# Optimization experiments

Measured on AMD Instinct MI355X. Metric: run time of the kernel, lower is better.

Reference implementation:

```python
import jax, jax.numpy as jnp
import numpy as np

N, D_IN, D_OUT, Q_DIM = 4096, 256, 256, 64


def _xavier(key, shape):
    fan_in, fan_out = shape[-2], shape[-1]
    bound = float(np.sqrt(6.0 / (fan_in + fan_out)))
    return jax.random.uniform(key, shape, jnp.float32, -bound, bound)


def setup_inputs() -> dict:
    key = jax.random.key(0)
    k_x, k_q, k_w, k_b = jax.random.split(key, 4)
    x = jax.random.normal(k_x, (N, D_IN), jnp.float32)
    query_vectors = jax.random.normal(k_q, (N, Q_DIM), jnp.float32)
    W_1 = _xavier(k_w, (Q_DIM, D_IN, D_OUT))  # xavier over last two dims (matches torch on 3D)
    b_1 = _xavier(k_b, (Q_DIM, D_OUT))
    return {"x": x, "query_vectors": query_vectors, "W_1": W_1, "b_1": b_1}


def reference(x, query_vectors, W_1, b_1):
    # Per-sample dynamic weight: W[n] = sum_d q[n,d] * W_1[d]; then x[n] @ W[n] + q[n] @ b_1.
    # Fused single contraction avoids materializing the [n, i, o] tensor; same math.
    out = jnp.einsum('ni,nd,dio->no', x, query_vectors, W_1)
    out = out + query_vectors @ b_1
    return out
```

## Files before the change

kernel.cpp:

```cpp
#include <hip/hip_runtime.h>
#include <stdint.h>


typedef _Float16 f16;
typedef f16 f16x8 __attribute__((ext_vector_type(8)));
typedef float f32x16 __attribute__((ext_vector_type(16)));

#define QDIM 64

#define XFRAG(DST, PTR)                                      \
  do {                                                       \
    float4 a_ = *(const float4*)(PTR);                       \
    float4 b_ = *(const float4*)((PTR) + 4);                 \
    f16x8 h_;                                                \
    h_[0] = (f16)a_.x; h_[1] = (f16)a_.y; h_[2] = (f16)a_.z; \
    h_[3] = (f16)a_.w; h_[4] = (f16)b_.x; h_[5] = (f16)b_.y; \
    h_[6] = (f16)b_.z; h_[7] = (f16)b_.w;                    \
    DST = h_;                                                \
  } while (0)

__global__ __launch_bounds__(256) void prep(const float* __restrict__ W,
                                            const float* __restrict__ B1,
                                            const float* __restrict__ X,
                                            f16* __restrict__ Wt,
                                            f16* __restrict__ Xt,
                                            f16* __restrict__ Bt) {
  const int b = blockIdx.x, t = threadIdx.x;
  if (b < 512) {
    const int d = b >> 3, grp = b & 7;
    const int ibL = t >> 6;
    const int ib = (grp << 2) + ibL;
    const int o0 = (t & 63) << 2;
    const int ic = ib >> 1, hb = ib & 1;
    float v[32];
#pragma unroll
    for (int j = 0; j < 8; ++j) {
      float4 f = *(const float4*)(W + ((size_t)d * 256 + (ib << 3) + j) * 256 + o0);
      v[j * 4 + 0] = f.x; v[j * 4 + 1] = f.y;
      v[j * 4 + 2] = f.z; v[j * 4 + 3] = f.w;
    }
#pragma unroll
    for (int oo = 0; oo < 4; ++oo) {
      const int o = o0 + oo, ncb = o >> 5, c = o & 31;
      f16x8 h;
#pragma unroll
      for (int j = 0; j < 8; ++j) h[j] = (f16)v[j * 4 + oo];
      *(f16x8*)((char*)Wt + ((((size_t)ncb * 64 + d) * 16 + ic) << 10) +
                (hb << 9) + (c << 4)) = h;
    }
  } else if (b < 576) {
    const int mb = b - 512;
#pragma unroll
    for (int rep = 0; rep < 8; ++rep) {
      const int u = (rep << 8) + t;
      const int row = u & 63, ish = u >> 6;
      const float* src = X + ((size_t)((mb << 6) + row)) * 256 + (ish << 3);
      f16x8 h;
      XFRAG(h, src);
      *(f16x8*)((char*)Xt + ((((size_t)mb * 16 + (ish >> 1)) * 2 + (ish & 1)) << 10) +
                (row << 4)) = h;
    }
  } else {
#pragma unroll
    for (int kb = 0; kb < 8; ++kb) {
      const float* src = B1 + ((size_t)kb << 3) * 256 + t;
      f16x8 h;
#pragma unroll
      for (int j = 0; j < 8; ++j) h[j] = (f16)src[(size_t)j << 8];
      *(f16x8*)((char*)Bt + (((size_t)(t >> 5) * 4 + (kb >> 1)) << 10) +
                ((kb & 1) << 9) + ((t & 31) << 4)) = h;
    }
  }
}

__global__ __launch_bounds__(256, 4) void mlp_main(const float* __restrict__ Q,
                                                   const f16* __restrict__ Wt,
                                                   const f16* __restrict__ Xt,
                                                   const f16* __restrict__ Bt,
                                                   float* __restrict__ out) {
  __shared__ __align__(16) float red[4][32][36];

  const int bid = blockIdx.x;
  const int nc = bid & 7;
  const int mb = bid >> 3;
  const int t = threadIdx.x;
  const int w = t >> 6;
  const int l = t & 63;
  const int l31 = l & 31;
  const int hf = l >> 5;

  const char* wl = (const char*)Wt + (((size_t)(nc * 64 + (w << 4))) << 14) +
                   (hf << 9) + (l31 << 4);
  const char* xb = (const char*)Xt + ((size_t)(mb >> 1) << 15) + (hf << 10) +
                   ((size_t)(((mb & 1) << 5) + l31) << 4);

  f16 qr[16];
  {
    const float* qp = Q + ((size_t)((mb << 5) + l31)) * QDIM + (w << 4);
#pragma unroll
    for (int g = 0; g < 4; ++g) {
      float4 v = *(const float4*)(qp + (g << 2));
      qr[g * 4 + 0] = (f16)v.x; qr[g * 4 + 1] = (f16)v.y;
      qr[g * 4 + 2] = (f16)v.z; qr[g * 4 + 3] = (f16)v.w;
    }
  }

  f32x16 acc[2];
#pragma unroll
  for (int p = 0; p < 2; ++p)
#pragma unroll
    for (int r = 0; r < 16; ++r) acc[p][r] = 0.f;

  f16x8 Wr[8], xfA, xfB;

  const int icoff = (((mb & 7) << 1) | (((mb >> 5) & 1) << 3)) & 15;

  xfA = *(const f16x8*)(xb + ((size_t)icoff << 11));
#pragma unroll
  for (int i = 0; i < 8; ++i)
    Wr[i] = *(const f16x8*)(wl + (((size_t)(i * 16 + icoff)) << 10));

  for (int s = 0; s < 16; ++s) {
    const int ic = (icoff + s) & 15;
    const int icn = (icoff + s + 1) & 15;
    xfB = *(const f16x8*)(xb + ((size_t)icn << 11));
#pragma unroll
    for (int i = 0; i < 8; ++i) {
      f16x8 wfr = Wr[i];
      Wr[i] = *(const f16x8*)(wl + (((size_t)((8 + i) * 16 + ic)) << 10));
      f16x8 a = xfA * qr[i];
      acc[i & 1] = __builtin_amdgcn_mfma_f32_32x32x16_f16(a, wfr, acc[i & 1], 0, 0, 0);
    }
#pragma unroll
    for (int i = 0; i < 8; ++i) {
      f16x8 wfr = Wr[i];
      Wr[i] = *(const f16x8*)(wl + (((size_t)(i * 16 + icn)) << 10));
      f16x8 a = xfA * qr[8 + i];
      acc[i & 1] = __builtin_amdgcn_mfma_f32_32x32x16_f16(a, wfr, acc[i & 1], 0, 0, 0);
    }
    xfA = xfB;
  }

#pragma unroll
  for (int r = 0; r < 16; ++r) acc[0][r] += acc[1][r];

  if (w == 0) {
#pragma unroll
    for (int kc = 0; kc < 4; ++kc) {
      f16x8 bf = *(const f16x8*)((const char*)Bt +
          (((size_t)nc * 4 + kc) << 10) + (hf << 9) + (l31 << 4));
      f16x8 q0;
      XFRAG(q0, Q + ((size_t)((mb << 5) + l31)) * QDIM + (kc << 4) + (hf << 3));
      acc[0] = __builtin_amdgcn_mfma_f32_32x32x16_f16(q0, bf, acc[0], 0, 0, 0);
    }
  }

#pragma unroll
  for (int r = 0; r < 16; ++r) {
    const int row0 = (r & 3) + ((r >> 2) << 3) + (hf << 2);
    red[w][row0][l31] = acc[0][r];
  }
  __syncthreads();

  const int row = t >> 3;
  const int cg = (t & 7) << 2;
  float4 sum = {0.f, 0.f, 0.f, 0.f};
#pragma unroll
  for (int wq = 0; wq < 4; ++wq) {
    float4 v = *(const float4*)(&red[wq][row][cg]);
    sum.x += v.x; sum.y += v.y; sum.z += v.z; sum.w += v.w;
  }
  *(float4*)(out + ((size_t)((mb << 5) + row)) * 256 + (nc << 5) + cg) = sum;
}

extern "C" void kernel_launch(void* const* d_in, const int* in_sizes, int n_in,
                              void* d_out, int out_size, void* d_ws, size_t ws_size,
                              hipStream_t stream) {
  (void)in_sizes; (void)n_in; (void)out_size; (void)ws_size;
  const float* x  = (const float*)d_in[0];
  const float* q  = (const float*)d_in[1];
  const float* W1 = (const float*)d_in[2];
  const float* b1 = (const float*)d_in[3];
  float* out = (float*)d_out;

  f16* Wt = (f16*)d_ws;
  f16* Bt = (f16*)((char*)d_ws + ((size_t)8 << 20));
  f16* Xt = (f16*)((char*)d_ws + ((size_t)8 << 20) + 32768);

  prep<<<577, 256, 0, stream>>>(W1, b1, x, Wt, Xt, Bt);
  mlp_main<<<1024, 256, 0, stream>>>(q, Wt, Xt, Bt, out);
}
```

Measured before the change: 133.1 us.

## Enlarge blocks to 1024 threads and reuse weight fragments across four row tiles

```diff
diff --git a/kernel.cpp b/kernel.cpp
--- a/kernel.cpp
+++ b/kernel.cpp
@@ -73,12 +73,12 @@
   }
 }
 
-__global__ __launch_bounds__(256, 4) void mlp_main(const float* __restrict__ Q,
-                                                   const f16* __restrict__ Wt,
-                                                   const f16* __restrict__ Xt,
-                                                   const f16* __restrict__ Bt,
-                                                   float* __restrict__ out) {
-  __shared__ __align__(16) float red[4][32][36];
+__global__ __launch_bounds__(1024, 4) void mlp_main(const float* __restrict__ Q,
+                                                    const f16* __restrict__ Wt,
+                                                    const f16* __restrict__ Xt,
+                                                    const f16* __restrict__ Bt,
+                                                    float* __restrict__ out) {
+  __shared__ __align__(16) float red[8][128][36];
 
   const int bid = blockIdx.x;
   const int nc = bid & 7;
@@ -89,88 +89,101 @@
   const int l31 = l & 31;
   const int hf = l >> 5;
 
-  const char* wl = (const char*)Wt + (((size_t)(nc * 64 + (w << 4))) << 14) +
+  const char* wl = (const char*)Wt + (((size_t)(nc * 64 + (w << 2))) << 14) +
                    (hf << 9) + (l31 << 4);
-  const char* xb = (const char*)Xt + ((size_t)(mb >> 1) << 15) + (hf << 10) +
-                   ((size_t)(((mb & 1) << 5) + l31) << 4);
-
-  f16 qr[16];
-  {
-    const float* qp = Q + ((size_t)((mb << 5) + l31)) * QDIM + (w << 4);
-#pragma unroll
-    for (int g = 0; g < 4; ++g) {
-      float4 v = *(const float4*)(qp + (g << 2));
-      qr[g * 4 + 0] = (f16)v.x; qr[g * 4 + 1] = (f16)v.y;
-      qr[g * 4 + 2] = (f16)v.z; qr[g * 4 + 3] = (f16)v.w;
-    }
-  }
-
-  f32x16 acc[2];
-#pragma unroll
-  for (int p = 0; p < 2; ++p)
-#pragma unroll
-    for (int r = 0; r < 16; ++r) acc[p][r] = 0.f;
-
-  f16x8 Wr[8], xfA, xfB;
-
-  const int icoff = (((mb & 7) << 1) | (((mb >> 5) & 1) << 3)) & 15;
-
-  xfA = *(const f16x8*)(xb + ((size_t)icoff << 11));
-#pragma unroll
-  for (int i = 0; i < 8; ++i)
-    Wr[i] = *(const f16x8*)(wl + (((size_t)(i * 16 + icoff)) << 10));
+  const char* xB = (const char*)Xt + ((size_t)(mb << 1) << 15) + (hf << 10) +
+                   ((size_t)l31 << 4);
+
+  f16 qr[4][4];
+#pragma unroll
+  for (int mt = 0; mt < 4; ++mt) {
+    float4 qv = *(const float4*)(Q + (size_t)((mb << 7) + (mt << 5) + l31) * QDIM +
+                                 (w << 2));
+    qr[mt][0] = (f16)qv.x; qr[mt][1] = (f16)qv.y;
+    qr[mt][2] = (f16)qv.z; qr[mt][3] = (f16)qv.w;
+  }
+
+  f32x16 acc[4];
+#pragma unroll
+  for (int mt = 0; mt < 4; ++mt)
+#pragma unroll
+    for (int r = 0; r < 16; ++r) acc[mt][r] = 0.f;
+
+  f16x8 Wr[4], xfA[4];
+
+  const int icoff = (mb & 7) << 1;
+
+#pragma unroll
+  for (int dd = 0; dd < 4; ++dd)
+    Wr[dd] = *(const f16x8*)(wl + (((size_t)((dd << 4) + icoff)) << 10));
+#pragma unroll
+  for (int mt = 0; mt < 4; ++mt)
+    xfA[mt] = *(const f16x8*)(xB + ((mt >> 1) << 15) + ((mt & 1) << 9) +
+                              ((size_t)icoff << 11));
 
   for (int s = 0; s < 16; ++s) {
-    const int ic = (icoff + s) & 15;
     const int icn = (icoff + s + 1) & 15;
-    xfB = *(const f16x8*)(xb + ((size_t)icn << 11));
-#pragma unroll
-    for (int i = 0; i < 8; ++i) {
-      f16x8 wfr = Wr[i];
-      Wr[i] = *(const f16x8*)(wl + (((size_t)((8 + i) * 16 + ic)) << 10));
-      f16x8 a = xfA * qr[i];
-      acc[i & 1] = __builtin_amdgcn_mfma_f32_32x32x16_f16(a, wfr, acc[i & 1], 0, 0, 0);
-    }
-#pragma unroll
-    for (int i = 0; i < 8; ++i) {
-      f16x8 wfr = Wr[i];
-      Wr[i] = *(const f16x8*)(wl + (((size_t)(i * 16 + icn)) << 10));
-      f16x8 a = xfA * qr[8 + i];
-      acc[i & 1] = __builtin_amdgcn_mfma_f32_32x32x16_f16(a, wfr, acc[i & 1], 0, 0, 0);
-    }
-    xfA = xfB;
-  }
-
-#pragma unroll
-  for (int r = 0; r < 16; ++r) acc[0][r] += acc[1][r];
-
-  if (w == 0) {
+#pragma unroll
+    for (int dd = 0; dd < 4; ++dd) {
+      f16x8 wf = Wr[dd];
+      Wr[dd] = *(const f16x8*)(wl + (((size_t)((dd << 4) + icn)) << 10));
+#pragma unroll
+      for (int mt = 0; mt < 4; ++mt) {
+        f16x8 a = xfA[mt] * qr[mt][dd];
+        acc[mt] = __builtin_amdgcn_mfma_f32_32x32x16_f16(a, wf, acc[mt], 0, 0, 0);
+      }
+    }
+#pragma unroll
+    for (int mt = 0; mt < 4; ++mt)
+      xfA[mt] = *(const f16x8*)(xB + ((mt >> 1) << 15) + ((mt & 1) << 9) +
+                                ((size_t)icn << 11));
+  }
+
+  if (w == 15) {
 #pragma unroll
     for (int kc = 0; kc < 4; ++kc) {
       f16x8 bf = *(const f16x8*)((const char*)Bt +
           (((size_t)nc * 4 + kc) << 10) + (hf << 9) + (l31 << 4));
-      f16x8 q0;
-      XFRAG(q0, Q + ((size_t)((mb << 5) + l31)) * QDIM + (kc << 4) + (hf << 3));
-      acc[0] = __builtin_amdgcn_mfma_f32_32x32x16_f16(q0, bf, acc[0], 0, 0, 0);
-    }
-  }
-
-#pragma unroll
-  for (int r = 0; r < 16; ++r) {
-    const int row0 = (r & 3) + ((r >> 2) << 3) + (hf << 2);
-    red[w][row0][l31] = acc[0][r];
+#pragma unroll
+      for (int mt = 0; mt < 4; ++mt) {
+        f16x8 qf;
+        XFRAG(qf, Q + (size_t)((mb << 7) + (mt << 5) + l31) * QDIM +
+                  (kc << 4) + (hf << 3));
+        acc[mt] = __builtin_amdgcn_mfma_f32_32x32x16_f16(qf, bf, acc[mt], 0, 0, 0);
+      }
+    }
+  }
+
+  if (w < 8) {
+#pragma unroll
+    for (int mt = 0; mt < 4; ++mt)
+#pragma unroll
+      for (int r = 0; r < 16; ++r) {
+        const int row = (mt << 5) + (r & 3) + ((r >> 2) << 3) + (hf << 2);
+        red[w][row][l31] = acc[mt][r];
+      }
   }
   __syncthreads();
-
-  const int row = t >> 3;
-  const int cg = (t & 7) << 2;
-  float4 sum = {0.f, 0.f, 0.f, 0.f};
-#pragma unroll
-  for (int wq = 0; wq < 4; ++wq) {
-    float4 v = *(const float4*)(&red[wq][row][cg]);
-    sum.x += v.x; sum.y += v.y; sum.z += v.z; sum.w += v.w;
-  }
-  *(float4*)(out + ((size_t)((mb << 5) + row)) * 256 + (nc << 5) + cg) = sum;
+  if (w >= 8) {
+#pragma unroll
+    for (int mt = 0; mt < 4; ++mt)
+#pragma unroll
+      for (int r = 0; r < 16; ++r) {
+        const int row = (mt << 5) + (r & 3) + ((r >> 2) << 3) + (hf << 2);
+        red[w - 8][row][l31] += acc[mt][r];
+      }
+  }
+  __syncthreads();
+
+  const int r = t >> 3;
+  const int c0 = (t & 7) << 2;
+  float4 s4 = {0.f, 0.f, 0.f, 0.f};
+#pragma unroll
+  for (int j = 0; j < 8; ++j) {
+    float4 v = *(const float4*)(&red[j][r][c0]);
+    s4.x += v.x; s4.y += v.y; s4.z += v.z; s4.w += v.w;
+  }
+  *(float4*)(out + ((size_t)((mb << 7) + r)) * 256 + (nc << 5) + c0) = s4;
 }
 
 extern "C" void kernel_launch(void* const* d_in, const int* in_sizes, int n_in,
@@ -188,5 +201,5 @@
   f16* Xt = (f16*)((char*)d_ws + ((size_t)8 << 20) + 32768);
 
   prep<<<577, 256, 0, stream>>>(W1, b1, x, Wt, Xt, Bt);
-  mlp_main<<<1024, 256, 0, stream>>>(q, Wt, Xt, Bt, out);
+  mlp_main<<<256, 1024, 0, stream>>>(q, Wt, Xt, Bt, out);
 }
```

New measurement: 402.4 us. 202% more time.

## Split Q-dim reduction across blocks with LDS-staged W tiles and separate reduce

Applied to the files above, without the earlier changes.

```diff
diff --git a/kernel.cpp b/kernel.cpp
--- a/kernel.cpp
+++ b/kernel.cpp
@@ -7,6 +7,13 @@
 typedef float f32x16 __attribute__((ext_vector_type(16)));
 
 #define QDIM 64
+
+__device__ __forceinline__ void gl_lds16(const void* g, void* s) {
+  __builtin_amdgcn_global_load_lds(
+      (const __attribute__((address_space(1))) void*)(uintptr_t)g,
+      (__attribute__((address_space(3))) void*)(uint32_t)(uintptr_t)s,
+      16, 0, 0);
+}
 
 #define XFRAG(DST, PTR)                                      \
   do {                                                       \
@@ -28,24 +35,18 @@
   const int b = blockIdx.x, t = threadIdx.x;
   if (b < 512) {
     const int d = b >> 3, grp = b & 7;
-    const int ibL = t >> 6;
-    const int ib = (grp << 2) + ibL;
-    const int o0 = (t & 63) << 2;
-    const int ic = ib >> 1, hb = ib & 1;
-    float v[32];
-#pragma unroll
-    for (int j = 0; j < 8; ++j) {
-      float4 f = *(const float4*)(W + ((size_t)d * 256 + (ib << 3) + j) * 256 + o0);
-      v[j * 4 + 0] = f.x; v[j * 4 + 1] = f.y;
-      v[j * 4 + 2] = f.z; v[j * 4 + 3] = f.w;
-    }
-#pragma unroll
-    for (int oo = 0; oo < 4; ++oo) {
-      const int o = o0 + oo, ncb = o >> 5, c = o & 31;
+#pragma unroll
+    for (int r = 0; r < 4; ++r) {
+      const int u = (r << 8) + t;
+      const int ibq = u >> 8;
+      const int o = u & 255;
+      const int ib = (grp << 2) + ibq;
       f16x8 h;
 #pragma unroll
-      for (int j = 0; j < 8; ++j) h[j] = (f16)v[j * 4 + oo];
-      *(f16x8*)((char*)Wt + ((((size_t)ncb * 64 + d) * 16 + ic) << 10) +
+      for (int j = 0; j < 8; ++j)
+        h[j] = (f16)W[((size_t)d * 256 + (ib << 3) + j) * 256 + o];
+      const int ncg = o >> 5, c = o & 31, ic = ib >> 1, hb = ib & 1;
+      *(f16x8*)((char*)Wt + ((((size_t)ncg * 64 + d) * 16 + ic) << 10) +
                 (hb << 9) + (c << 4)) = h;
     }
   } else if (b < 576) {
@@ -73,104 +74,141 @@
   }
 }
 
-__global__ __launch_bounds__(256, 4) void mlp_main(const float* __restrict__ Q,
+__global__ __launch_bounds__(512, 2) void mlp_main(const float* __restrict__ Q,
                                                    const f16* __restrict__ Wt,
                                                    const f16* __restrict__ Xt,
                                                    const f16* __restrict__ Bt,
-                                                   float* __restrict__ out) {
-  __shared__ __align__(16) float red[4][32][36];
+                                                   float* __restrict__ P) {
+  __shared__ __align__(16) char sw0[16384];
+  __shared__ __align__(16) char sw1[16384];
 
   const int bid = blockIdx.x;
-  const int nc = bid & 7;
-  const int mb = bid >> 3;
+  const int nc = bid & 3;
+  const int ks = (bid >> 2) & 7;
+  const int mb = bid >> 5;
   const int t = threadIdx.x;
   const int w = t >> 6;
+  const int wn = w & 1;
+  const int wm = w >> 1;
   const int l = t & 63;
   const int l31 = l & 31;
   const int hf = l >> 5;
 
-  const char* wl = (const char*)Wt + (((size_t)(nc * 64 + (w << 4))) << 14) +
-                   (hf << 9) + (l31 << 4);
-  const char* xb = (const char*)Xt + ((size_t)(mb >> 1) << 15) + (hf << 10) +
-                   ((size_t)(((mb & 1) << 5) + l31) << 4);
-
-  f16 qr[16];
+  const int dlo = ks << 3;
+  const int st = mb & 7;
+
+  const char* gW = (const char*)Wt + ((size_t)nc << 21) + (l << 4);
+
+  const char* xB = (const char*)Xt + ((size_t)((mb << 2) + wm) << 15) +
+                   (hf << 10) + (l31 << 4);
+
+  f16 qr0[8], qr1[8];
   {
-    const float* qp = Q + ((size_t)((mb << 5) + l31)) * QDIM + (w << 4);
-#pragma unroll
-    for (int g = 0; g < 4; ++g) {
-      float4 v = *(const float4*)(qp + (g << 2));
-      qr[g * 4 + 0] = (f16)v.x; qr[g * 4 + 1] = (f16)v.y;
-      qr[g * 4 + 2] = (f16)v.z; qr[g * 4 + 3] = (f16)v.w;
-    }
-  }
-
-  f32x16 acc[2];
-#pragma unroll
-  for (int p = 0; p < 2; ++p)
-#pragma unroll
-    for (int r = 0; r < 16; ++r) acc[p][r] = 0.f;
-
-  f16x8 Wr[8], xfA, xfB;
-
-  const int icoff = (((mb & 7) << 1) | (((mb >> 5) & 1) << 3)) & 15;
-
-  xfA = *(const f16x8*)(xb + ((size_t)icoff << 11));
-#pragma unroll
-  for (int i = 0; i < 8; ++i)
-    Wr[i] = *(const f16x8*)(wl + (((size_t)(i * 16 + icoff)) << 10));
-
-  for (int s = 0; s < 16; ++s) {
-    const int ic = (icoff + s) & 15;
-    const int icn = (icoff + s + 1) & 15;
-    xfB = *(const f16x8*)(xb + ((size_t)icn << 11));
-#pragma unroll
-    for (int i = 0; i < 8; ++i) {
-      f16x8 wfr = Wr[i];
-      Wr[i] = *(const f16x8*)(wl + (((size_t)((8 + i) * 16 + ic)) << 10));
-      f16x8 a = xfA * qr[i];
-      acc[i & 1] = __builtin_amdgcn_mfma_f32_32x32x16_f16(a, wfr, acc[i & 1], 0, 0, 0);
-    }
-#pragma unroll
-    for (int i = 0; i < 8; ++i) {
-      f16x8 wfr = Wr[i];
-      Wr[i] = *(const f16x8*)(wl + (((size_t)(i * 16 + icn)) << 10));
-      f16x8 a = xfA * qr[8 + i];
-      acc[i & 1] = __builtin_amdgcn_mfma_f32_32x32x16_f16(a, wfr, acc[i & 1], 0, 0, 0);
-    }
-    xfA = xfB;
-  }
-
-#pragma unroll
-  for (int r = 0; r < 16; ++r) acc[0][r] += acc[1][r];
-
-  if (w == 0) {
+    const float* qp0 = Q + ((size_t)((mb << 8) + (wm << 6) + l31)) * QDIM + dlo;
+    const float* qp1 = qp0 + (size_t)32 * QDIM;
+#pragma unroll
+    for (int dt = 0; dt < 8; ++dt) {
+      qr0[dt] = (f16)qp0[(dt + st) & 7];
+      qr1[dt] = (f16)qp1[(dt + st) & 7];
+    }
+  }
+
+  f32x16 acc0, acc1;
+#pragma unroll
+  for (int r = 0; r < 16; ++r) { acc0[r] = 0.f; acc1[r] = 0.f; }
+
+  f16x8 xf[16];
+
+#define STAGE2(H, DABS, SBUF)                                              \
+  do {                                                                     \
+    gl_lds16(gW + ((size_t)(DABS) << 14) + ((((H) << 3) + w) << 10),       \
+             (SBUF) + ((w << 1) << 10) + (l << 4));                        \
+    gl_lds16(gW + ((size_t)1 << 20) + ((size_t)(DABS) << 14) +             \
+                 ((((H) << 3) + w) << 10),                                 \
+             (SBUF) + (((w << 1) + 1) << 10) + (l << 4));                  \
+  } while (0)
+
+#define LOADXF(H)                                                          \
+  do {                                                                     \
+    _Pragma("unroll")                                                      \
+    for (int k2 = 0; k2 < 8; ++k2) {                                       \
+      xf[k2 * 2 + 0] = *(const f16x8*)(xB + ((((H) << 3) + k2) << 11));    \
+      xf[k2 * 2 + 1] =                                                     \
+          *(const f16x8*)(xB + ((((H) << 3) + k2) << 11) + (1 << 9));      \
+    }                                                                      \
+  } while (0)
+
+#define CSTEP(DT, SBUF)                                                    \
+  do {                                                                     \
+    const f16 qa_ = qr0[DT], qb_ = qr1[DT];                                \
+    _Pragma("unroll")                                                      \
+    for (int k2 = 0; k2 < 8; ++k2) {                                       \
+      f16x8 bf_ = *(const f16x8*)((SBUF) + (((k2 << 1) | wn) << 10) +      \
+                                  (l << 4));                               \
+      acc0 = __builtin_amdgcn_mfma_f32_32x32x16_f16(xf[k2 * 2 + 0] * qa_,  \
+                                                    bf_, acc0, 0, 0, 0);   \
+      acc1 = __builtin_amdgcn_mfma_f32_32x32x16_f16(xf[k2 * 2 + 1] * qb_,  \
+                                                    bf_, acc1, 0, 0, 0);   \
+    }                                                                      \
+  } while (0)
+
+  STAGE2(0, dlo + (st & 7), sw0);
+  LOADXF(0);
+  __syncthreads();
+
+#pragma unroll
+  for (int h = 0; h < 2; ++h) {
+#pragma unroll
+    for (int dt = 0; dt < 8; ++dt) {
+      const int step = (h << 3) + dt;
+      if (step < 15) {
+        const int hn = (step + 1) >> 3, dtn = (step + 1) & 7;
+        const int dabs = dlo + ((dtn + st) & 7);
+        if (step & 1) STAGE2(hn, dabs, sw0); else STAGE2(hn, dabs, sw1);
+      }
+      if (step & 1) CSTEP(dt, sw1); else CSTEP(dt, sw0);
+      __syncthreads();
+    }
+    if (h == 0) LOADXF(1);
+  }
+
+  if (ks == 0) {
+    const int ncg = (nc << 1) + wn;
 #pragma unroll
     for (int kc = 0; kc < 4; ++kc) {
       f16x8 bf = *(const f16x8*)((const char*)Bt +
-          (((size_t)nc * 4 + kc) << 10) + (hf << 9) + (l31 << 4));
-      f16x8 q0;
-      XFRAG(q0, Q + ((size_t)((mb << 5) + l31)) * QDIM + (kc << 4) + (hf << 3));
-      acc[0] = __builtin_amdgcn_mfma_f32_32x32x16_f16(q0, bf, acc[0], 0, 0, 0);
-    }
-  }
-
+          (((size_t)ncg * 4 + kc) << 10) + (hf << 9) + (l31 << 4));
+      f16x8 q0, q1;
+      XFRAG(q0, Q + ((size_t)((mb << 8) + (wm << 6) + l31)) * QDIM +
+                (kc << 4) + (hf << 3));
+      XFRAG(q1, Q + ((size_t)((mb << 8) + (wm << 6) + 32 + l31)) * QDIM +
+                (kc << 4) + (hf << 3));
+      acc0 = __builtin_amdgcn_mfma_f32_32x32x16_f16(q0, bf, acc0, 0, 0, 0);
+      acc1 = __builtin_amdgcn_mfma_f32_32x32x16_f16(q1, bf, acc1, 0, 0, 0);
+    }
+  }
+
+  float* Pg = P + ((size_t)ks << 20);
+  const int colg = (nc << 6) + (wn << 5) + l31;
+  const int rbase = (mb << 8) + (wm << 6);
 #pragma unroll
   for (int r = 0; r < 16; ++r) {
-    const int row0 = (r & 3) + ((r >> 2) << 3) + (hf << 2);
-    red[w][row0][l31] = acc[0][r];
-  }
-  __syncthreads();
-
-  const int row = t >> 3;
-  const int cg = (t & 7) << 2;
-  float4 sum = {0.f, 0.f, 0.f, 0.f};
-#pragma unroll
-  for (int wq = 0; wq < 4; ++wq) {
-    float4 v = *(const float4*)(&red[wq][row][cg]);
-    sum.x += v.x; sum.y += v.y; sum.z += v.z; sum.w += v.w;
-  }
-  *(float4*)(out + ((size_t)((mb << 5) + row)) * 256 + (nc << 5) + cg) = sum;
+    const int rr = (r & 3) + ((r >> 2) << 3) + (hf << 2);
+    Pg[(size_t)(rbase + rr) * 256 + colg] = acc0[r];
+    Pg[(size_t)(rbase + 32 + rr) * 256 + colg] = acc1[r];
+  }
+}
+
+__global__ __launch_bounds__(256) void reduce8(const float* __restrict__ P,
+                                               float* __restrict__ out) {
+  const size_t i = (((size_t)blockIdx.x << 8) + threadIdx.x) << 2;
+  float4 s = *(const float4*)(P + i);
+#pragma unroll
+  for (int g = 1; g < 8; ++g) {
+    float4 v = *(const float4*)(P + ((size_t)g << 20) + i);
+    s.x += v.x; s.y += v.y; s.z += v.z; s.w += v.w;
+  }
+  *(float4*)(out + i) = s;
 }
 
 extern "C" void kernel_launch(void* const* d_in, const int* in_sizes, int n_in,
@@ -186,7 +224,9 @@
   f16* Wt = (f16*)d_ws;
   f16* Bt = (f16*)((char*)d_ws + ((size_t)8 << 20));
   f16* Xt = (f16*)((char*)d_ws + ((size_t)8 << 20) + 32768);
+  float* P = (float*)((char*)d_ws + ((size_t)8 << 20) + 32768 + ((size_t)2 << 20));
 
   prep<<<577, 256, 0, stream>>>(W1, b1, x, Wt, Xt, Bt);
-  mlp_main<<<1024, 256, 0, stream>>>(q, Wt, Xt, Bt, out);
-}
+  mlp_main<<<512, 512, 0, stream>>>(q, Wt, Xt, Bt, P);
+  reduce8<<<1024, 256, 0, stream>>>(P, out);
+}
```

Result: faster. 128.8 us (-3.2%).
